# Performance work log

Hardware: AMD Instinct MI355X
Metric: run time of the kernel (lower is better)

Reference implementation:

```python
import jax, jax.numpy as jnp
import numpy as np

T, DIM, H = 1024, 2048, 16
QLR, KVLR = 1024, 512
NOPE, ROPE, VD = 128, 64, 128
QKD = NOPE + ROPE          # 192
IH, ID, TOPK = 16, 128, 256
EPS = 1e-6

def rmsnorm(x, w):
    return x * jax.lax.rsqrt(jnp.mean(x * x, axis=-1, keepdims=True) + EPS) * w

def layernorm(x, w, b, eps=1e-5):
    m = jnp.mean(x, axis=-1, keepdims=True)
    v = jnp.mean((x - m) ** 2, axis=-1, keepdims=True)
    return (x - m) * jax.lax.rsqrt(v + eps) * w + b

def apply_rope(x, cos, sin):
    # non-interleaved: first half = real, second half = imag
    d = x.shape[-1] // 2
    while cos.ndim < x.ndim:
        cos, sin = cos[:, None], sin[:, None]
    x1, x2 = x[..., :d], x[..., d:]
    return jnp.concatenate([x1 * cos - x2 * sin, x1 * sin + x2 * cos], axis=-1)

def hadamard(x):
    # unnormalized Walsh-Hadamard on last dim (power of 2)
    n = x.shape[-1]
    shape = x.shape
    y, h = x, 1
    while h < n:
        y = y.reshape(shape[:-1] + (-1, 2 * h))
        a, b = y[..., :h], y[..., h:]
        y = jnp.concatenate([a + b, a - b], axis=-1)
        h *= 2
    return y.reshape(shape)

def rotate_activation(x):
    # half-swap then Hadamard on each half
    d = x.shape[-1] // 2
    x1, x2 = x[..., :d], x[..., d:]
    return jnp.concatenate([hadamard(x2), hadamard(x1)], axis=-1)

def setup_inputs() -> dict:
    key = jax.random.key(0)
    ks = jax.random.split(key, 10)
    s = 0.02
    w = lambda k, shp: jax.random.normal(k, shp, jnp.float32) * s
    pos = jnp.arange(T, dtype=jnp.float32)
    inv = 1.0 / (10000.0 ** (jnp.arange(0, ROPE, 2, dtype=jnp.float32) / ROPE))
    ang = pos[:, None] * inv[None, :]
    return {
        'hidden_states': jax.random.normal(ks[0], (T, DIM), jnp.float32),
        'rope_cos': jnp.cos(ang), 'rope_sin': jnp.sin(ang),
        'wq_a': w(ks[1], (QLR, DIM)),
        'q_norm_w': jnp.ones((QLR,), jnp.float32),
        'wq_b': w(ks[2], (H * QKD, QLR)),
        'wkv_a': w(ks[3], (KVLR + ROPE, DIM)),
        'kv_norm_w': jnp.ones((KVLR,), jnp.float32),
        'wkv_b': w(ks[4], (H * (NOPE + VD), KVLR)),
        'wo': w(ks[5], (DIM, H * VD)),
        'iq_norm_w': jnp.ones((QLR,), jnp.float32),
        'iwq_b': w(ks[6], (IH * ID, QLR)),
        'iwk': w(ks[7], (IH * ID, DIM)),
        'k_norm_w': jnp.ones((ID,), jnp.float32),
        'k_norm_b': jnp.zeros((ID,), jnp.float32),
        'wproj': w(ks[8], (IH, DIM)),
    }

def reference(hidden_states, rope_cos, rope_sin, wq_a, q_norm_w, wq_b,
              wkv_a, kv_norm_w, wkv_b, wo, iq_norm_w, iwq_b, iwk,
              k_norm_w, k_norm_b, wproj):
    x = hidden_states
    t = x.shape[0]
    qr = x @ wq_a.T                                   # [t, QLR]

    # ---- lightning indexer: top-k causal token selection ----
    iq = (rmsnorm(qr, iq_norm_w) @ iwq_b.T).reshape(t, IH, ID)
    iq = jnp.concatenate([apply_rope(iq[..., :ROPE], rope_cos, rope_sin), iq[..., ROPE:]], -1)
    iq = rotate_activation(iq)
    ik = layernorm((x @ iwk.T).reshape(t, IH, ID), k_norm_w, k_norm_b)
    ik = jnp.concatenate([apply_rope(ik[..., :ROPE], rope_cos, rope_sin), ik[..., ROPE:]], -1)
    ik = rotate_activation(ik)
    w = (x @ wproj.T) * (IH ** -0.5) * (ID ** -0.5)   # [t, IH]
    dots = jax.nn.relu(jnp.einsum('thd,shd->ths', iq, ik)) * w[:, :, None]
    score = dots.sum(axis=1)                          # [t, t]
    rows = jnp.arange(t)
    score = jnp.where(rows[None, :] <= rows[:, None], score, -jnp.inf)
    _, topk_idx = jax.lax.top_k(score, TOPK)          # [t, TOPK]
    valid = topk_idx <= rows[:, None]
    safe_idx = jnp.where(valid, topk_idx, 0)

    # ---- MLA latent projections ----
    q = (rmsnorm(qr, q_norm_w) @ wq_b.T).reshape(t, H, QKD)
    q_nope, q_pe = q[..., :NOPE], q[..., NOPE:]
    q_pe = apply_rope(q_pe, rope_cos, rope_sin)
    kv_a = x @ wkv_a.T                                # [t, KVLR+ROPE]
    kv = rmsnorm(kv_a[:, :KVLR], kv_norm_w)
    k_pe = apply_rope(kv_a[:, KVLR:], rope_cos, rope_sin)
    wkv = wkv_b.reshape(H, NOPE + VD, KVLR)
    w_k, w_v = wkv[:, :NOPE, :], wkv[:, NOPE:, :]
    q_nope_proj = jnp.einsum('thd,hdc->thc', q_nope, w_k)
    q_key = jnp.concatenate([q_nope_proj, q_pe], -1)  # [t, H, KVLR+ROPE]
    kv_key = jnp.concatenate([kv, k_pe], -1)          # [t, KVLR+ROPE]

    # ---- sparse attention over selected indices ----
    sel = kv_key[safe_idx]                            # [t, TOPK, KVLR+ROPE]
    scale = QKD ** -0.5
    logits = jnp.einsum('thc,tkc->thk', q_key, sel) * scale
    logits = jnp.where(valid[:, None, :], logits, -jnp.inf)
    attn = jax.nn.softmax(logits, axis=-1)
    out_latent = jnp.einsum('thk,tkc->thc', attn, sel[..., :KVLR])
    out_v = jnp.einsum('thc,hdc->thd', out_latent, w_v)
    return out_v.reshape(t, H * VD) @ wo.T            # [t, DIM]
```

## Files before the change

kernel.cpp:

```cpp
#include <hip/hip_runtime.h>
#include <hip/hip_bf16.h>
#include <math.h>

#define T_     1024
#define DIM_   2048
#define H_     16
#define QLR_   1024
#define KVLR_  512
#define NOPE_  128
#define ROPE_  64
#define VD_    128
#define QKD_   192
#define IH_    16
#define ID_    128
#define TOPK_  256
#define CKV_   576

#define SCALE_W    0.022097086912079608f
#define SCALE_LOG  0.07216878364870323f

typedef short bfrag __attribute__((ext_vector_type(8)));
typedef float ffrag __attribute__((ext_vector_type(4)));

__device__ __forceinline__ unsigned short f2bf(float f) {
    union { __hip_bfloat16 h; unsigned short u; } c; c.h = __float2bfloat16(f); return c.u;
}
__device__ __forceinline__ float bf2f(unsigned short u) {
    union { unsigned short u; __hip_bfloat16 h; } c; c.u = u; return __bfloat162float(c.h);
}

struct CastSeg { const float* src; unsigned short* hi; unsigned short* lo; };
struct CastDesc { CastSeg seg[6]; int bstart[7]; int nseg; };

__global__ __launch_bounds__(256) void castm_k(CastDesc d)
{
    int b = blockIdx.x, s = 0;
    #pragma unroll
    for (int i = 1; i < 6; ++i) if (i < d.nseg && b >= d.bstart[i]) s = i;
    long base = ((long)(b - d.bstart[s]) * 256 + threadIdx.x) * 4;
    float4 v = *(const float4*)(d.seg[s].src + base);
    ushort4 h4;
    h4.x = f2bf(v.x); h4.y = f2bf(v.y); h4.z = f2bf(v.z); h4.w = f2bf(v.w);
    *(ushort4*)(d.seg[s].hi + base) = h4;
    if (d.seg[s].lo) {
        ushort4 l4;
        l4.x = f2bf(v.x - bf2f(h4.x));
        l4.y = f2bf(v.y - bf2f(h4.y));
        l4.z = f2bf(v.z - bf2f(h4.z));
        l4.w = f2bf(v.w - bf2f(h4.w));
        *(ushort4*)(d.seg[s].lo + base) = l4;
    }
}

__global__ __launch_bounds__(256) void qrnorm_k(const float* __restrict__ qr,
    const float* __restrict__ iqw, const float* __restrict__ qw,
    unsigned short* __restrict__ qriq_hi, unsigned short* __restrict__ qriq_lo,
    unsigned short* __restrict__ qrq_hi)
{
    int t = blockIdx.x, tid = threadIdx.x;
    long base = (long)t * QLR_ + tid * 4;
    float4 v = *(const float4*)(qr + base);
    __shared__ float red[256];
    red[tid] = v.x * v.x + v.y * v.y + v.z * v.z + v.w * v.w;
    __syncthreads();
    for (int off = 128; off; off >>= 1) { if (tid < off) red[tid] += red[tid + off]; __syncthreads(); }
    float r = rsqrtf(red[0] / (float)QLR_ + 1e-6f);
    int col = tid * 4;
    float4 wi = *(const float4*)(iqw + col);
    float4 wq = *(const float4*)(qw + col);
    float s[4] = {v.x, v.y, v.z, v.w};
    float wiv[4] = {wi.x, wi.y, wi.z, wi.w};
    float wqv[4] = {wq.x, wq.y, wq.z, wq.w};
    ushort4 h4, l4, g4;
    unsigned short* hp = (unsigned short*)&h4;
    unsigned short* lp = (unsigned short*)&l4;
    unsigned short* gp = (unsigned short*)&g4;
    #pragma unroll
    for (int i = 0; i < 4; ++i) {
        float ai = s[i] * wiv[i] * r;
        float aq = s[i] * wqv[i] * r;
        hp[i] = f2bf(ai);
        lp[i] = f2bf(ai - bf2f(hp[i]));
        gp[i] = f2bf(aq);
    }
    *(ushort4*)(qriq_hi + base) = h4;
    *(ushort4*)(qriq_lo + base) = l4;
    *(ushort4*)(qrq_hi + base) = g4;
}

__global__ __launch_bounds__(256) void gemm_bt_mfma_k(
    const unsigned short* __restrict__ A, const unsigned short* __restrict__ B,
    void* __restrict__ Cv, long sA, long sB, long sC,
    int lda, int ldb, int ldc, int N, int K, int obf)
{
    A += (long)blockIdx.z * sA;
    B += (long)blockIdx.z * sB;
    __shared__ unsigned short As[128 * 40];
    __shared__ unsigned short Bs[128 * 40];
    const int tid = threadIdx.x;
    const int bm = blockIdx.y * 128, bn = blockIdx.x * 128;
    const int wave = tid >> 6, lane = tid & 63;
    const int wm = (wave >> 1) * 64, wn = (wave & 1) * 64;
    const int lm = lane & 15, quad = lane >> 4;

    ffrag acc[4][4];
    #pragma unroll
    for (int mi = 0; mi < 4; ++mi)
        #pragma unroll
        for (int ni = 0; ni < 4; ++ni)
            #pragma unroll
            for (int r = 0; r < 4; ++r) acc[mi][ni][r] = 0.f;

    const int srow = tid >> 1, shalf = tid & 1;
    const long aoff = (long)(bm + srow) * lda + shalf * 16;
    int brow = bn + srow; if (brow > N - 1) brow = N - 1;
    const long boff = (long)brow * ldb + shalf * 16;
    unsigned short* la = As + srow * 40 + shalf * 16;
    unsigned short* lb = Bs + srow * 40 + shalf * 16;

    uint4 va0 = *(const uint4*)(A + aoff);
    uint4 va1 = *(const uint4*)(A + aoff + 8);
    uint4 vb0 = *(const uint4*)(B + boff);
    uint4 vb1 = *(const uint4*)(B + boff + 8);

    for (int k0 = 0; k0 < K; k0 += 32) {
        __syncthreads();
        *(uint4*)la = va0; *(uint4*)(la + 8) = va1;
        *(uint4*)lb = vb0; *(uint4*)(lb + 8) = vb1;
        __syncthreads();
        if (k0 + 32 < K) {
            va0 = *(const uint4*)(A + aoff + k0 + 32);
            va1 = *(const uint4*)(A + aoff + k0 + 40);
            vb0 = *(const uint4*)(B + boff + k0 + 32);
            vb1 = *(const uint4*)(B + boff + k0 + 40);
        }
        bfrag af[4], bf[4];
        #pragma unroll
        for (int mi = 0; mi < 4; ++mi)
            af[mi] = *(const bfrag*)(As + (wm + mi * 16 + lm) * 40 + quad * 8);
        #pragma unroll
        for (int ni = 0; ni < 4; ++ni)
            bf[ni] = *(const bfrag*)(Bs + (wn + ni * 16 + lm) * 40 + quad * 8);
        #pragma unroll
        for (int mi = 0; mi < 4; ++mi)
            #pragma unroll
            for (int ni = 0; ni < 4; ++ni)
                acc[mi][ni] = __builtin_amdgcn_mfma_f32_16x16x32_bf16(
                    af[mi], bf[ni], acc[mi][ni], 0, 0, 0);
    }

    #pragma unroll
    for (int mi = 0; mi < 4; ++mi)
        #pragma unroll
        for (int ni = 0; ni < 4; ++ni) {
            int n = bn + wn + ni * 16 + lm;
            if (n < N) {
                int mb = bm + wm + mi * 16 + quad * 4;
                if (obf) {
                    unsigned short* C = (unsigned short*)Cv + (long)blockIdx.z * sC;
                    #pragma unroll
                    for (int r = 0; r < 4; ++r)
                        C[(long)(mb + r) * ldc + n] = f2bf(acc[mi][ni][r]);
                } else {
                    float* C = (float*)Cv + (long)blockIdx.z * sC;
                    #pragma unroll
                    for (int r = 0; r < 4; ++r)
                        C[(long)(mb + r) * ldc + n] = acc[mi][ni][r];
                }
            }
        }
}

struct GSeg {
    const void* A; const void* Al; const void* B; const void* Bl;
    void* C; void* C2;
    long sA, sB, sC;
    int lda, ldb, ldc, N, K, bnx, bmx, mode, obf;
};
struct GDesc { GSeg seg[4]; int bstart[5]; int nseg; };

__global__ __launch_bounds__(256) void mgemm_k(GDesc d)
{
    __shared__ unsigned short Ahs[64 * 72], Als[64 * 72], Bhs[64 * 72], Bls[64 * 72];
    const int tid = threadIdx.x;
    const int b = blockIdx.x;
    int s = 0;
    #pragma unroll
    for (int i = 1; i < 4; ++i) if (i < d.nseg && b >= d.bstart[i]) s = i;
    const int rel = b - d.bstart[s];
    const int mode = d.seg[s].mode;

    if (mode == 2) {
        const float* src = (const float*)d.seg[s].A;
        unsigned short* hi = (unsigned short*)d.seg[s].C;
        unsigned short* lo = (unsigned short*)d.seg[s].C2;
        long base = ((long)rel * 256 + tid) * 4;
        float4 v = *(const float4*)(src + base);
        ushort4 h4;
        h4.x = f2bf(v.x); h4.y = f2bf(v.y); h4.z = f2bf(v.z); h4.w = f2bf(v.w);
        *(ushort4*)(hi + base) = h4;
        if (lo) {
            ushort4 l4;
            l4.x = f2bf(v.x - bf2f(h4.x));
            l4.y = f2bf(v.y - bf2f(h4.y));
            l4.z = f2bf(v.z - bf2f(h4.z));
            l4.w = f2bf(v.w - bf2f(h4.w));
            *(ushort4*)(lo + base) = l4;
        }
        return;
    }
    if (mode == 3) {
        const float* x = (const float*)d.seg[s].A;
        const float* wproj = (const float*)d.seg[s].B;
        float* wt = (float*)d.seg[s].C;
        float* xs = (float*)Ahs;
        int t = rel;
        for (int c = tid; c < DIM_; c += 256) xs[c] = x[(long)t * DIM_ + c];
        __syncthreads();
        int wave = tid >> 6, lane = tid & 63;
        #pragma unroll
        for (int i = 0; i < 4; ++i) {
            int h = wave * 4 + i;
            float sum = 0.f;
            for (int c = lane; c < DIM_; c += 64) sum += xs[c] * wproj[(long)h * DIM_ + c];
            for (int off = 32; off; off >>= 1) sum += __shfl_xor(sum, off, 64);
            if (lane == 0) wt[(long)t * IH_ + h] = sum * SCALE_W;
        }
        return;
    }
    if (mode == 4) {
        const float* in = (const float*)d.seg[s].A;
        unsigned short* out = (unsigned short*)d.seg[s].C;
        int h = rel >> 6, c0 = (rel & 15) * 32, d0 = ((rel >> 4) & 3) * 32;
        float (*tt)[33] = (float(*)[33])(void*)Ahs;
        int tx = tid & 31, ty = tid >> 5;
        #pragma unroll
        for (int i = 0; i < 4; ++i)
            tt[ty + i * 8][tx] = in[(long)(h * 256 + d0 + ty + i * 8) * 512 + c0 + tx];
        __syncthreads();
        #pragma unroll
        for (int i = 0; i < 4; ++i)
            out[((long)h * 512 + c0 + ty + i * 8) * 128 + d0 + tx] = f2bf(tt[tx][ty + i * 8]);
        return;
    }
    if (mode == 5) {
        const float* q = (const float*)d.seg[s].A;
        const float* cosb = (const float*)d.seg[s].B;
        const float* sinb = (const float*)d.seg[s].Bl;
        unsigned short* qk = (unsigned short*)d.seg[s].C;
        int row = rel * 8 + (tid >> 5);
        int i = tid & 31;
        int t = row / H_;
        const float* qp = q + (long)row * QKD_ + NOPE_;
        float x1 = qp[i], x2 = qp[i + 32];
        float c = cosb[t * 32 + i], sn = sinb[t * 32 + i];
        unsigned short* o = qk + (long)row * CKV_ + 512;
        o[i]      = f2bf(x1 * c - x2 * sn);
        o[i + 32] = f2bf(x1 * sn + x2 * c);
        return;
    }

    const GSeg g = d.seg[s];
    const bool three = (mode == 1);
    const int per = g.bnx * g.bmx;
    const int z = rel / per;
    const int r2 = rel - z * per;
    const int bm = (r2 / g.bnx) * 64, bn = (r2 % g.bnx) * 64;
    const unsigned short* A  = (const unsigned short*)g.A + (long)z * g.sA;
    const unsigned short* B  = (const unsigned short*)g.B + (long)z * g.sB;
    const unsigned short* Alp = (const unsigned short*)g.Al;
    const unsigned short* Blp = (const unsigned short*)g.Bl;

    const int wave = tid >> 6, lane = tid & 63;
    const int wm = (wave >> 1) * 32, wn = (wave & 1) * 32;
    const int lm = lane & 15, quad = lane >> 4;

    ffrag acc[2][2];
    #pragma unroll
    for (int mi = 0; mi < 2; ++mi)
        #pragma unroll
        for (int ni = 0; ni < 2; ++ni)
            #pragma unroll
            for (int r = 0; r < 4; ++r) acc[mi][ni][r] = 0.f;

    const int srow = tid >> 2, schunk = tid & 3;
    const long aoff = (long)(bm + srow) * g.lda + schunk * 8;
    int brow = bn + srow; if (brow > g.N - 1) brow = g.N - 1;
    const long boff = (long)brow * g.ldb + schunk * 8;
    const int loff = srow * 72 + schunk * 8;

    uint4 va0, va1, vb0, vb1, wa0, wa1, wb0, wb1;
    va0 = *(const uint4*)(A + aoff);
    va1 = *(const uint4*)(A + aoff + 32);
    vb0 = *(const uint4*)(B + boff);
    vb1 = *(const uint4*)(B + boff + 32);
    if (three) {
        wa0 = *(const uint4*)(Alp + aoff);
        wa1 = *(const uint4*)(Alp + aoff + 32);
        wb0 = *(const uint4*)(Blp + boff);
        wb1 = *(const uint4*)(Blp + boff + 32);
    }

    for (int k0 = 0; k0 < g.K; k0 += 64) {
        __syncthreads();
        *(uint4*)(Ahs + loff) = va0; *(uint4*)(Ahs + loff + 32) = va1;
        *(uint4*)(Bhs + loff) = vb0; *(uint4*)(Bhs + loff + 32) = vb1;
        if (three) {
            *(uint4*)(Als + loff) = wa0; *(uint4*)(Als + loff + 32) = wa1;
            *(uint4*)(Bls + loff) = wb0; *(uint4*)(Bls + loff + 32) = wb1;
        }
        __syncthreads();
        if (k0 + 64 < g.K) {
            va0 = *(const uint4*)(A + aoff + k0 + 64);
            va1 = *(const uint4*)(A + aoff + k0 + 96);
            vb0 = *(const uint4*)(B + boff + k0 + 64);
            vb1 = *(const uint4*)(B + boff + k0 + 96);
            if (three) {
                wa0 = *(const uint4*)(Alp + aoff + k0 + 64);
                wa1 = *(const uint4*)(Alp + aoff + k0 + 96);
                wb0 = *(const uint4*)(Blp + boff + k0 + 64);
                wb1 = *(const uint4*)(Blp + boff + k0 + 96);
            }
        }
        bfrag ah[2][2], bh[2][2], al[2][2], bl[2][2];
        #pragma unroll
        for (int mi = 0; mi < 2; ++mi)
            #pragma unroll
            for (int ks = 0; ks < 2; ++ks)
                ah[mi][ks] = *(const bfrag*)(Ahs + (wm + mi * 16 + lm) * 72 + ks * 32 + quad * 8);
        #pragma unroll
        for (int ni = 0; ni < 2; ++ni)
            #pragma unroll
            for (int ks = 0; ks < 2; ++ks)
                bh[ni][ks] = *(const bfrag*)(Bhs + (wn + ni * 16 + lm) * 72 + ks * 32 + quad * 8);
        if (three) {
            #pragma unroll
            for (int mi = 0; mi < 2; ++mi)
                #pragma unroll
                for (int ks = 0; ks < 2; ++ks)
                    al[mi][ks] = *(const bfrag*)(Als + (wm + mi * 16 + lm) * 72 + ks * 32 + quad * 8);
            #pragma unroll
            for (int ni = 0; ni < 2; ++ni)
                #pragma unroll
                for (int ks = 0; ks < 2; ++ks)
                    bl[ni][ks] = *(const bfrag*)(Bls + (wn + ni * 16 + lm) * 72 + ks * 32 + quad * 8);
        }
        #pragma unroll
        for (int mi = 0; mi < 2; ++mi)
            #pragma unroll
            for (int ni = 0; ni < 2; ++ni) {
                acc[mi][ni] = __builtin_amdgcn_mfma_f32_16x16x32_bf16(ah[mi][0], bh[ni][0], acc[mi][ni], 0, 0, 0);
                if (three) {
                    acc[mi][ni] = __builtin_amdgcn_mfma_f32_16x16x32_bf16(ah[mi][0], bl[ni][0], acc[mi][ni], 0, 0, 0);
                    acc[mi][ni] = __builtin_amdgcn_mfma_f32_16x16x32_bf16(al[mi][0], bh[ni][0], acc[mi][ni], 0, 0, 0);
                }
                acc[mi][ni] = __builtin_amdgcn_mfma_f32_16x16x32_bf16(ah[mi][1], bh[ni][1], acc[mi][ni], 0, 0, 0);
                if (three) {
                    acc[mi][ni] = __builtin_amdgcn_mfma_f32_16x16x32_bf16(ah[mi][1], bl[ni][1], acc[mi][ni], 0, 0, 0);
                    acc[mi][ni] = __builtin_amdgcn_mfma_f32_16x16x32_bf16(al[mi][1], bh[ni][1], acc[mi][ni], 0, 0, 0);
                }
            }
    }

    #pragma unroll
    for (int mi = 0; mi < 2; ++mi)
        #pragma unroll
        for (int ni = 0; ni < 2; ++ni) {
            int n = bn + wn + ni * 16 + lm;
            if (n < g.N) {
                int mb = bm + wm + mi * 16 + quad * 4;
                if (g.obf) {
                    unsigned short* C = (unsigned short*)g.C + (long)z * g.sC;
                    #pragma unroll
                    for (int r = 0; r < 4; ++r)
                        C[(long)(mb + r) * g.ldc + n] = f2bf(acc[mi][ni][r]);
                } else {
                    float* C = (float*)g.C + (long)z * g.sC;
                    #pragma unroll
                    for (int r = 0; r < 4; ++r)
                        C[(long)(mb + r) * g.ldc + n] = acc[mi][ni][r];
                }
            }
        }
}

__global__ __launch_bounds__(256) void mtrans_k(
    const float* __restrict__ iq, unsigned short* __restrict__ iqh, unsigned short* __restrict__ iql,
    const float* __restrict__ ik, unsigned short* __restrict__ ikh, unsigned short* __restrict__ ikl,
    const float* __restrict__ knw, const float* __restrict__ knb,
    const float* __restrict__ kva, unsigned short* __restrict__ kvb, const float* __restrict__ kvnw,
    const float* __restrict__ cosb, const float* __restrict__ sinb)
{
    __shared__ float red[256];
    __shared__ float rsh;
    const int b = blockIdx.x, tid = threadIdx.x;
    if (b < 8192) {
        const bool isq = b < 4096;
        int rb = isq ? b : b - 4096;
        int row = rb * 4 + (tid >> 6);
        int p = tid & 63;
        int t = row >> 4;
        const float* src = isq ? iq : ik;
        float a = src[(long)row * 128 + p];
        float bb = src[(long)row * 128 + 64 + p];
        if (!isq) {
            float ssum = a + bb;
            #pragma unroll
            for (int o = 1; o < 64; o <<= 1) ssum += __shfl_xor(ssum, o, 64);
            float m = ssum * (1.f / 128.f);
            float da = a - m, db = bb - m;
            float v = da * da + db * db;
            #pragma unroll
            for (int o = 1; o < 64; o <<= 1) v += __shfl_xor(v, o, 64);
            float r = rsqrtf(v * (1.f / 128.f) + 1e-5f);
            a = da * r * knw[p] + knb[p];
            bb = db * r * knw[64 + p] + knb[64 + p];
        }
        float c = cosb[t * 32 + (p & 31)], sn = sinb[t * 32 + (p & 31)];
        float asw = __shfl_xor(a, 32, 64);
        a = (p < 32) ? (a * c - asw * sn) : (asw * sn + a * c);
        #pragma unroll
        for (int h = 1; h < 64; h <<= 1) {
            float a2 = __shfl_xor(a, h, 64);
            float b2 = __shfl_xor(bb, h, 64);
            a = (p & h) ? (a2 - a) : (a + a2);
            bb = (p & h) ? (b2 - bb) : (bb + b2);
        }
        unsigned short* hi = isq ? iqh : ikh;
        unsigned short* lo = isq ? iql : ikl;
        unsigned short hb = f2bf(bb), ha = f2bf(a);
        hi[(long)row * 128 + p] = hb;
        hi[(long)row * 128 + 64 + p] = ha;
        lo[(long)row * 128 + p] = f2bf(bb - bf2f(hb));
        lo[(long)row * 128 + 64 + p] = f2bf(a - bf2f(ha));
    } else {
        int t = b - 8192;
        const float* a = kva + (long)t * CKV_;
        unsigned short* o = kvb + (long)t * CKV_;
        float v0 = a[tid], v1 = a[tid + 256];
        red[tid] = v0 * v0 + v1 * v1; __syncthreads();
        for (int off = 128; off; off >>= 1) { if (tid < off) red[tid] += red[tid + off]; __syncthreads(); }
        if (tid == 0) rsh = rsqrtf(red[0] / (float)KVLR_ + 1e-6f);
        __syncthreads();
        float rs = rsh;
        o[tid]       = f2bf(v0 * rs * kvnw[tid]);
        o[tid + 256] = f2bf(v1 * rs * kvnw[tid + 256]);
        if (tid < 32) {
            float x1 = a[512 + tid], x2 = a[544 + tid];
            float c = cosb[t * 32 + tid], sn = sinb[t * 32 + tid];
            o[512 + tid] = f2bf(x1 * c - x2 * sn);
            o[544 + tid] = f2bf(x1 * sn + x2 * c);
        }
    }
}

__global__ __launch_bounds__(256) void score3_k(
    const unsigned short* __restrict__ iqh, const unsigned short* __restrict__ iql,
    const unsigned short* __restrict__ ikh, const unsigned short* __restrict__ ikl,
    const float* __restrict__ wtok, float* __restrict__ score)
{
    const int bt = blockIdx.y, bs = blockIdx.x;
    if (bs > bt) return;
    __shared__ unsigned short Ah[64 * 72], Al[64 * 72], Bh[64 * 72], Bl[64 * 72];
    __shared__ float wts[64][16];
    const int tid = threadIdx.x;
    const int wave = tid >> 6, lane = tid & 63;
    const int wm = (wave >> 1) * 32, wn = (wave & 1) * 32;
    const int lm = lane & 15, quad = lane >> 4;
    const int t0 = bt * 64, s0 = bs * 64;
    const int srow = tid >> 2, schunk = tid & 3;
    const int loff = srow * 72 + schunk * 8;

    for (int e = tid; e < 1024; e += 256)
        wts[e >> 4][e & 15] = wtok[(long)(t0 + (e >> 4)) * IH_ + (e & 15)];

    const long abase = (long)(t0 + srow) * 2048 + schunk * 8;
    const long bbase = (long)(s0 + srow) * 2048 + schunk * 8;

    uint4 pah0 = *(const uint4*)(iqh + abase);
    uint4 pah1 = *(const uint4*)(iqh + abase + 32);
    uint4 pal0 = *(const uint4*)(iql + abase);
    uint4 pal1 = *(const uint4*)(iql + abase + 32);
    uint4 pbh0 = *(const uint4*)(ikh + bbase);
    uint4 pbh1 = *(const uint4*)(ikh + bbase + 32);
    uint4 pbl0 = *(const uint4*)(ikl + bbase);
    uint4 pbl1 = *(const uint4*)(ikl + bbase + 32);

    float accf[2][2][4] = {};

    for (int h = 0; h < IH_; ++h) {
        ffrag acch[2][2];
        #pragma unroll
        for (int mi = 0; mi < 2; ++mi)
            #pragma unroll
            for (int ni = 0; ni < 2; ++ni)
                #pragma unroll
                for (int r = 0; r < 4; ++r) acch[mi][ni][r] = 0.f;

        #pragma unroll
        for (int k0 = 0; k0 < ID_; k0 += 64) {
            __syncthreads();
            *(uint4*)(Ah + loff) = pah0; *(uint4*)(Ah + loff + 32) = pah1;
            *(uint4*)(Al + loff) = pal0; *(uint4*)(Al + loff + 32) = pal1;
            *(uint4*)(Bh + loff) = pbh0; *(uint4*)(Bh + loff + 32) = pbh1;
            *(uint4*)(Bl + loff) = pbl0; *(uint4*)(Bl + loff + 32) = pbl1;
            __syncthreads();
            int step = h * 2 + (k0 >> 6) + 1;
            if (step < 32) {
                int off = (step >> 1) * 128 + (step & 1) * 64;
                pah0 = *(const uint4*)(iqh + abase + off);
                pah1 = *(const uint4*)(iqh + abase + off + 32);
                pal0 = *(const uint4*)(iql + abase + off);
                pal1 = *(const uint4*)(iql + abase + off + 32);
                pbh0 = *(const uint4*)(ikh + bbase + off);
                pbh1 = *(const uint4*)(ikh + bbase + off + 32);
                pbl0 = *(const uint4*)(ikl + bbase + off);
                pbl1 = *(const uint4*)(ikl + bbase + off + 32);
            }
            bfrag ahf[2][2], alf[2][2], bhf[2][2], blf[2][2];
            #pragma unroll
            for (int mi = 0; mi < 2; ++mi)
                #pragma unroll
                for (int ks = 0; ks < 2; ++ks) {
                    ahf[mi][ks] = *(const bfrag*)(Ah + (wm + mi * 16 + lm) * 72 + ks * 32 + quad * 8);
                    alf[mi][ks] = *(const bfrag*)(Al + (wm + mi * 16 + lm) * 72 + ks * 32 + quad * 8);
                }
            #pragma unroll
            for (int ni = 0; ni < 2; ++ni)
                #pragma unroll
                for (int ks = 0; ks < 2; ++ks) {
                    bhf[ni][ks] = *(const bfrag*)(Bh + (wn + ni * 16 + lm) * 72 + ks * 32 + quad * 8);
                    blf[ni][ks] = *(const bfrag*)(Bl + (wn + ni * 16 + lm) * 72 + ks * 32 + quad * 8);
                }
            #pragma unroll
            for (int mi = 0; mi < 2; ++mi)
                #pragma unroll
                for (int ni = 0; ni < 2; ++ni) {
                    acch[mi][ni] = __builtin_amdgcn_mfma_f32_16x16x32_bf16(ahf[mi][0], bhf[ni][0], acch[mi][ni], 0, 0, 0);
                    acch[mi][ni] = __builtin_amdgcn_mfma_f32_16x16x32_bf16(ahf[mi][0], blf[ni][0], acch[mi][ni], 0, 0, 0);
                    acch[mi][ni] = __builtin_amdgcn_mfma_f32_16x16x32_bf16(alf[mi][0], bhf[ni][0], acch[mi][ni], 0, 0, 0);
                    acch[mi][ni] = __builtin_amdgcn_mfma_f32_16x16x32_bf16(ahf[mi][1], bhf[ni][1], acch[mi][ni], 0, 0, 0);
                    acch[mi][ni] = __builtin_amdgcn_mfma_f32_16x16x32_bf16(ahf[mi][1], blf[ni][1], acch[mi][ni], 0, 0, 0);
                    acch[mi][ni] = __builtin_amdgcn_mfma_f32_16x16x32_bf16(alf[mi][1], bhf[ni][1], acch[mi][ni], 0, 0, 0);
                }
        }
        #pragma unroll
        for (int mi = 0; mi < 2; ++mi) {
            float wr[4];
            #pragma unroll
            for (int r = 0; r < 4; ++r) wr[r] = wts[wm + mi * 16 + quad * 4 + r][h];
            #pragma unroll
            for (int ni = 0; ni < 2; ++ni)
                #pragma unroll
                for (int r = 0; r < 4; ++r)
                    accf[mi][ni][r] += fmaxf(acch[mi][ni][r], 0.f) * wr[r];
        }
    }
    #pragma unroll
    for (int mi = 0; mi < 2; ++mi)
        #pragma unroll
        for (int ni = 0; ni < 2; ++ni) {
            int s = s0 + wn + ni * 16 + lm;
            int tb = t0 + wm + mi * 16 + quad * 4;
            #pragma unroll
            for (int r = 0; r < 4; ++r)
                score[(long)(tb + r) * T_ + s] = accf[mi][ni][r];
        }
}

__global__ __launch_bounds__(512) void topk_k(const float* __restrict__ score, int* __restrict__ topk)
{
    int t = blockIdx.x, tid = threadIdx.x;
    __shared__ float v[1024];
    __shared__ int ix[1024];
    for (int i = tid; i < 1024; i += 512) {
        v[i] = (i <= t) ? score[(long)t * T_ + i] : -INFINITY;
        ix[i] = i;
    }
    __syncthreads();
    for (int k = 2; k <= 1024; k <<= 1) {
        for (int j = k >> 1; j > 0; j >>= 1) {
            for (int i = tid; i < 1024; i += 512) {
                int l = i ^ j;
                if (l > i) {
                    bool up = ((i & k) == 0);
                    float vi = v[i], vl = v[l];
                    int xi = ix[i], xl = ix[l];
                    bool iBetter = (vi > vl) || (vi == vl && xi < xl);
                    bool doSwap = up ? !iBetter : iBetter;
                    if (doSwap) { v[i] = vl; v[l] = vi; ix[i] = xl; ix[l] = xi; }
                }
            }
            __syncthreads();
        }
    }
    if (tid < 256) topk[(long)t * TOPK_ + tid] = ix[tid];
}

__global__ __launch_bounds__(256, 4) void attn3_k(
    const unsigned short* __restrict__ qkeyb, const unsigned short* __restrict__ kvb,
    const int* __restrict__ topkp, unsigned short* __restrict__ olat)
{
    __shared__ __align__(16) unsigned short U[13568];
    __shared__ float red[16 * 17];
    __shared__ int kidx[256];
    unsigned short* Qbf = U;
    float*          Lg  = (float*)U;
    unsigned short* VT0 = U;
    unsigned short* VT1 = U + 4608;
    unsigned short* Pbf = U + 9344;

    const int t = blockIdx.x, tid = threadIdx.x;
    const int wave = tid >> 6, lane = tid & 63;
    const int lm = lane & 15, quad = lane >> 4;

    kidx[tid] = topkp[(long)t * TOPK_ + tid];
    const uint2* q2 = (const uint2*)(qkeyb + (long)t * (H_ * CKV_));
    #pragma unroll
    for (int rep = 0; rep < 9; ++rep) {
        int e = rep * 256 + tid;
        uint2 v = q2[e];
        int f = e * 4, h = f / CKV_, c = f - h * CKV_;
        *(uint2*)(Qbf + h * 584 + c) = v;
    }
    int myk0 = topkp[(long)t * TOPK_ + wave * 64 + 0 * 16 + lm];
    int myk1 = topkp[(long)t * TOPK_ + wave * 64 + 1 * 16 + lm];
    int myk2 = topkp[(long)t * TOPK_ + wave * 64 + 2 * 16 + lm];
    int myk3 = topkp[(long)t * TOPK_ + wave * 64 + 3 * 16 + lm];
    __syncthreads();

    ffrag acc[4];
    #pragma unroll
    for (int ni = 0; ni < 4; ++ni)
        #pragma unroll
        for (int r = 0; r < 4; ++r) acc[ni][r] = 0.f;

    const unsigned short* kb0 = kvb + (long)myk0 * CKV_ + quad * 8;
    const unsigned short* kb1 = kvb + (long)myk1 * CKV_ + quad * 8;
    const unsigned short* kb2 = kvb + (long)myk2 * CKV_ + quad * 8;
    const unsigned short* kb3 = kvb + (long)myk3 * CKV_ + quad * 8;

    bfrag ba[4], bb[4], bc[4];
    #define LDT(DST, C) { \
        DST[0] = *(const bfrag*)(kb0 + (C)); \
        DST[1] = *(const bfrag*)(kb1 + (C)); \
        DST[2] = *(const bfrag*)(kb2 + (C)); \
        DST[3] = *(const bfrag*)(kb3 + (C)); }
    #define PHA_STEP(I, BUF) { \
        bfrag af = *(const bfrag*)(Qbf + lm * 584 + (I) * 32 + quad * 8); \
        _Pragma("unroll") \
        for (int ni = 0; ni < 4; ++ni) \
            acc[ni] = __builtin_amdgcn_mfma_f32_16x16x32_bf16(af, BUF[ni], acc[ni], 0, 0, 0); \
        if ((I) < 15) LDT(BUF, (I) * 32 + 96) }

    LDT(ba, 0) LDT(bb, 32) LDT(bc, 64)
    PHA_STEP(0, ba)  PHA_STEP(1, bb)  PHA_STEP(2, bc)
    PHA_STEP(3, ba)  PHA_STEP(4, bb)  PHA_STEP(5, bc)
    PHA_STEP(6, ba)  PHA_STEP(7, bb)  PHA_STEP(8, bc)
    PHA_STEP(9, ba)  PHA_STEP(10, bb) PHA_STEP(11, bc)
    PHA_STEP(12, ba) PHA_STEP(13, bb) PHA_STEP(14, bc)
    PHA_STEP(15, ba) PHA_STEP(16, bb) PHA_STEP(17, bc)
    #undef PHA_STEP
    #undef LDT

    __syncthreads();
    #pragma unroll
    for (int ni = 0; ni < 4; ++ni)
        #pragma unroll
        for (int r = 0; r < 4; ++r)
            Lg[(quad * 4 + r) * 260 + wave * 64 + ni * 16 + lm] = acc[ni][r];
    __syncthreads();

    {
        int h = tid >> 4, j = tid & 15;
        float m = -INFINITY;
        #pragma unroll
        for (int kk = 0; kk < 16; ++kk) {
            int key = j * 16 + kk;
            if (kidx[key] <= t) m = fmaxf(m, Lg[h * 260 + key]);
        }
        red[h * 17 + j] = m;
        __syncthreads();
        float mh = -INFINITY;
        #pragma unroll
        for (int jj = 0; jj < 16; ++jj) mh = fmaxf(mh, red[h * 17 + jj]);
        __syncthreads();
        float s = 0.f;
        float pv[16];
        #pragma unroll
        for (int kk = 0; kk < 16; ++kk) {
            int key = j * 16 + kk;
            float e = (kidx[key] <= t) ? expf(Lg[h * 260 + key] * SCALE_LOG - mh * SCALE_LOG) : 0.f;
            pv[kk] = e; s += e;
        }
        red[h * 17 + j] = s;
        __syncthreads();
        float sh = 0.f;
        #pragma unroll
        for (int jj = 0; jj < 16; ++jj) sh += red[h * 17 + jj];
        float inv = 1.f / sh;
        #pragma unroll
        for (int kk = 0; kk < 16; ++kk)
            Pbf[h * 264 + j * 16 + kk] = f2bf(pv[kk] * inv);
    }

    const int kpair = tid & 15, cgrp = tid >> 4;
    ffrag acc2[2];
    #pragma unroll
    for (int ci = 0; ci < 2; ++ci)
        #pragma unroll
        for (int r = 0; r < 4; ++r) acc2[ci][r] = 0.f;

    uint4 ga0, gb0, ga1, gb1;
    #define PREFB(GA, GB, IT) { \
        int ka_ = kidx[((IT) & 7) * 32 + 2 * kpair]; \
        int kb_ = kidx[((IT) & 7) * 32 + 2 * kpair + 1]; \
        long co_ = (long)(((IT) >> 3) * 128 + cgrp * 8); \
        GA = *(const uint4*)(kvb + (long)ka_ * CKV_ + co_); \
        GB = *(const uint4*)(kvb + (long)kb_ * CKV_ + co_); }
    #define STOREB(GA, GB, BUF) { \
        const unsigned short* pa_ = (const unsigned short*)&GA; \
        const unsigned short* pb_ = (const unsigned short*)&GB; \
        _Pragma("unroll") \
        for (int i_ = 0; i_ < 8; ++i_) \
            *(unsigned int*)((BUF) + (cgrp * 8 + i_) * 36 + 2 * kpair) = \
                (unsigned int)pa_[i_] | ((unsigned int)pb_[i_] << 16); }
    #define MFMAB(BUF, IT) { \
        bfrag pa = *(const bfrag*)(Pbf + lm * 264 + ((IT) & 7) * 32 + quad * 8); \
        _Pragma("unroll") \
        for (int ci = 0; ci < 2; ++ci) { \
            int c = wave * 32 + ci * 16 + lm; \
            bfrag bv; \
            ((uint2*)&bv)[0] = *(const uint2*)((BUF) + c * 36 + quad * 8); \
            ((uint2*)&bv)[1] = *(const uint2*)((BUF) + c * 36 + quad * 8 + 4); \
            acc2[ci] = __builtin_amdgcn_mfma_f32_16x16x32_bf16(pa, bv, acc2[ci], 0, 0, 0); } }
    #define OLATST(IT) { \
        int p_ = (IT) >> 3; \
        _Pragma("unroll") \
        for (int ci = 0; ci < 2; ++ci) \
            _Pragma("unroll") \
            for (int r = 0; r < 4; ++r) \
                olat[((long)t * H_ + quad * 4 + r) * 512 + p_ * 128 + wave * 32 + ci * 16 + lm] \
                    = f2bf(acc2[ci][r]); \
        _Pragma("unroll") \
        for (int ci = 0; ci < 2; ++ci) \
            _Pragma("unroll") \
            for (int r = 0; r < 4; ++r) acc2[ci][r] = 0.f; }
    #define LGKBAR() { asm volatile("s_waitcnt lgkmcnt(0)" ::: "memory"); \
                       __builtin_amdgcn_s_barrier(); }

    PREFB(ga0, gb0, 0);
    PREFB(ga1, gb1, 1);
    LGKBAR();
    STOREB(ga0, gb0, VT0);
    LGKBAR();
    for (int it = 0; it < 32; it += 2) {
        STOREB(ga1, gb1, VT1);
        MFMAB(VT0, it);
        if (it + 2 < 32) PREFB(ga0, gb0, it + 2);
        LGKBAR();
        if (it + 2 < 32) STOREB(ga0, gb0, VT0);
        MFMAB(VT1, it + 1);
        if (it + 3 < 32) PREFB(ga1, gb1, it + 3);
        if (((it + 1) & 7) == 7) OLATST(it + 1);
        LGKBAR();
    }
    #undef PREFB
    #undef STOREB
    #undef MFMAB
    #undef OLATST
    #undef LGKBAR
}

extern "C" void kernel_launch(void* const* d_in, const int* in_sizes, int n_in,
                              void* d_out, int out_size, void* d_ws, size_t ws_size,
                              hipStream_t stream)
{
    const float* x          = (const float*)d_in[0];
    const float* cosb       = (const float*)d_in[1];
    const float* sinb       = (const float*)d_in[2];
    const float* wq_a       = (const float*)d_in[3];
    const float* q_norm_w   = (const float*)d_in[4];
    const float* wq_b       = (const float*)d_in[5];
    const float* wkv_a      = (const float*)d_in[6];
    const float* kv_norm_w  = (const float*)d_in[7];
    const float* wkv_b      = (const float*)d_in[8];
    const float* wo         = (const float*)d_in[9];
    const float* iq_norm_w  = (const float*)d_in[10];
    const float* iwq_b      = (const float*)d_in[11];
    const float* iwk        = (const float*)d_in[12];
    const float* k_norm_w   = (const float*)d_in[13];
    const float* k_norm_b   = (const float*)d_in[14];
    const float* wproj      = (const float*)d_in[15];
    float* out = (float*)d_out;

    float* ws    = (float*)d_ws;
    float* qr    = ws;
    float* wtok  = ws + 1049600;
    int*   topk  = (int*)(ws + 1655808);
    float* qkey  = ws + 1917952;
    float* outv  = ws + 11355136;
    float* U0    = ws + 13452288;
    float* iq    = U0;
    float* ik    = U0 + 2097152;
    float* kva   = U0 + 4194304;
    float* qbuf  = U0 + 4784128;
    float* score = U0 + 7929856;

    unsigned short* qkey_u = (unsigned short*)qkey;
    unsigned short* wqa_hi  = qkey_u;
    unsigned short* wqa_lo  = qkey_u + 2097152;
    unsigned short* iwk_hi  = qkey_u + 4194304;
    unsigned short* iwk_lo  = qkey_u + 8388608;
    unsigned short* iwqb_hi = qkey_u + 12582912;
    unsigned short* iwqb_lo = qkey_u + 14680064;
    unsigned short* qriq_hi = qkey_u + 16777216;
    unsigned short* qriq_lo = qkey_u + 17825792;
    unsigned short* iqbf_hi = qkey_u;
    unsigned short* iqbf_lo = qkey_u + 2097152;
    unsigned short* ikbf_hi = qkey_u + 4194304;
    unsigned short* ikbf_lo = qkey_u + 6291456;
    unsigned short* qkey_bf = qkey_u;
    unsigned short* wkvb_bf = qkey_u + 9437184;
    unsigned short* wo_bf   = qkey_u;
    unsigned short* q_u     = (unsigned short*)qbuf;
    unsigned short* x_hi    = q_u;
    unsigned short* x_lo    = q_u + 2097152;
    unsigned short* wkva_hi = q_u + 4194304;
    unsigned short* outv_u  = (unsigned short*)outv;
    unsigned short* wqb_hi  = outv_u;
    unsigned short* qrq_hi  = outv_u + 3145728;
    unsigned short* outv_bf = outv_u;
    unsigned short* qbf     = (unsigned short*)iq;
    unsigned short* wkT     = (unsigned short*)ik;
    unsigned short* kvb     = (unsigned short*)qr;
    unsigned short* olat_bf = (unsigned short*)U0;

    {
        CastDesc d;
        d.seg[0] = { x,      x_hi,    x_lo    };
        d.seg[1] = { wq_a,   wqa_hi,  wqa_lo  };
        d.seg[2] = { iwk,    iwk_hi,  iwk_lo  };
        d.seg[3] = { iwq_b,  iwqb_hi, iwqb_lo };
        d.seg[4] = { wkv_a,  wkva_hi, nullptr };
        d.seg[5] = { wq_b,   wqb_hi,  nullptr };
        d.bstart[0] = 0;     d.bstart[1] = 2048;  d.bstart[2] = 4096;
        d.bstart[3] = 8192;  d.bstart[4] = 10240; d.bstart[5] = 11392;
        d.bstart[6] = 14464; d.nseg = 6;
        castm_k<<<14464, 256, 0, stream>>>(d);
    }

    {
        GDesc d{};
        d.nseg = 3;
        d.bstart[0] = 0; d.bstart[1] = 256; d.bstart[2] = 768; d.bstart[3] = 1792;
        GSeg& s0 = d.seg[0];
        s0.A = x_hi; s0.Al = x_lo; s0.B = wqa_hi; s0.Bl = wqa_lo; s0.C = qr;
        s0.lda = DIM_; s0.ldb = DIM_; s0.ldc = QLR_; s0.N = QLR_; s0.K = DIM_;
        s0.bnx = 16; s0.bmx = 16; s0.mode = 1; s0.obf = 0;
        GSeg& s1 = d.seg[1];
        s1.A = x_hi; s1.Al = x_lo; s1.B = iwk_hi; s1.Bl = iwk_lo; s1.C = ik;
        s1.lda = DIM_; s1.ldb = DIM_; s1.ldc = IH_ * ID_; s1.N = IH_ * ID_; s1.K = DIM_;
        s1.bnx = 32; s1.bmx = 16; s1.mode = 1; s1.obf = 0;
        GSeg& s2 = d.seg[2];
        s2.A = x; s2.B = wproj; s2.C = wtok; s2.mode = 3;
        mgemm_k<<<1792, 256, 0, stream>>>(d);
    }

    qrnorm_k<<<T_, 256, 0, stream>>>(qr, iq_norm_w, q_norm_w, qriq_hi, qriq_lo, qrq_hi);

    {
        GDesc d{};
        d.nseg = 3;
        d.bstart[0] = 0; d.bstart[1] = 512; d.bstart[2] = 656; d.bstart[3] = 2704;
        GSeg& s0 = d.seg[0];
        s0.A = qriq_hi; s0.Al = qriq_lo; s0.B = iwqb_hi; s0.Bl = iwqb_lo; s0.C = iq;
        s0.lda = QLR_; s0.ldb = QLR_; s0.ldc = IH_ * ID_; s0.N = IH_ * ID_; s0.K = QLR_;
        s0.bnx = 32; s0.bmx = 16; s0.mode = 1; s0.obf = 0;
        GSeg& s1 = d.seg[1];
        s1.A = x_hi; s1.B = wkva_hi; s1.C = kva;
        s1.lda = DIM_; s1.ldb = DIM_; s1.ldc = CKV_; s1.N = CKV_; s1.K = DIM_;
        s1.bnx = 9; s1.bmx = 16; s1.mode = 0; s1.obf = 0;
        GSeg& s2 = d.seg[2];
        s2.A = wkv_b; s2.C = wkvb_bf; s2.C2 = nullptr; s2.mode = 2;
        mgemm_k<<<2704, 256, 0, stream>>>(d);
    }

    {
        GDesc d{};
        d.nseg = 1;
        d.bstart[0] = 0; d.bstart[1] = 768;
        GSeg& s0 = d.seg[0];
        s0.A = qrq_hi; s0.B = wqb_hi; s0.C = qbuf;
        s0.lda = QLR_; s0.ldb = QLR_; s0.ldc = H_ * QKD_; s0.N = H_ * QKD_; s0.K = QLR_;
        s0.bnx = 48; s0.bmx = 16; s0.mode = 0; s0.obf = 0;
        mgemm_k<<<768, 256, 0, stream>>>(d);
    }

    mtrans_k<<<9216, 256, 0, stream>>>(iq, iqbf_hi, iqbf_lo, ik, ikbf_hi, ikbf_lo,
                                       k_norm_w, k_norm_b, kva, kvb, kv_norm_w, cosb, sinb);

    score3_k<<<dim3(T_/64, T_/64), 256, 0, stream>>>(iqbf_hi, iqbf_lo, ikbf_hi, ikbf_lo, wtok, score);
    topk_k<<<T_, 512, 0, stream>>>(score, topk);

    {
        GDesc d{};
        d.nseg = 3;
        d.bstart[0] = 0; d.bstart[1] = 3072; d.bstart[2] = 4096; d.bstart[3] = 6144;
        GSeg& s0 = d.seg[0];
        s0.A = qbuf; s0.C = qbf; s0.C2 = nullptr; s0.mode = 2;
        GSeg& s1 = d.seg[1];
        s1.A = wkv_b; s1.C = wkT; s1.mode = 4;
        GSeg& s2 = d.seg[2];
        s2.A = qbuf; s2.B = cosb; s2.Bl = sinb; s2.C = qkey_bf; s2.mode = 5;
        mgemm_k<<<6144, 256, 0, stream>>>(d);
    }

    gemm_bt_mfma_k<<<dim3(KVLR_/128, T_/128, H_), 256, 0, stream>>>(
        qbf, wkT, qkey_bf, 192L, 65536L, 576L, H_*QKD_, ID_, H_*CKV_, KVLR_, ID_, 1);

    attn3_k<<<T_, 256, 0, stream>>>(qkey_bf, kvb, topk, olat_bf);

    {
        GDesc d{};
        d.nseg = 2;
        d.bstart[0] = 0; d.bstart[1] = 512; d.bstart[2] = 4608;
        GSeg& s0 = d.seg[0];
        s0.A = olat_bf; s0.B = wkvb_bf + (long)NOPE_ * KVLR_; s0.C = outv_bf;
        s0.sA = 512; s0.sB = (long)(NOPE_ + VD_) * KVLR_; s0.sC = VD_;
        s0.lda = H_ * KVLR_; s0.ldb = KVLR_; s0.ldc = H_ * VD_; s0.N = VD_; s0.K = KVLR_;
        s0.bnx = 2; s0.bmx = 16; s0.mode = 0; s0.obf = 1;
        GSeg& s1 = d.seg[1];
        s1.A = wo; s1.C = wo_bf; s1.C2 = nullptr; s1.mode = 2;
        mgemm_k<<<4608, 256, 0, stream>>>(d);
    }

    {
        GDesc d{};
        d.nseg = 1;
        d.bstart[0] = 0; d.bstart[1] = 512;
        GSeg& s0 = d.seg[0];
        s0.A = outv_bf; s0.B = wo_bf; s0.C = out;
        s0.lda = H_ * VD_; s0.ldb = H_ * VD_; s0.ldc = DIM_; s0.N = DIM_; s0.K = H_ * VD_;
        s0.bnx = 32; s0.bmx = 16; s0.mode = 0; s0.obf = 0;
        mgemm_k<<<512, 256, 0, stream>>>(d);
    }

    (void)in_sizes; (void)n_in; (void)out_size; (void)ws_size;
}
```

Measured before the change: 494.3 us.

## Split indexer score kernel across head groups and sum partials in top-k

The indexer score kernel gains a grid z-dimension of 4, so each block handles 4 of the 16 indexer heads. Each block writes a partial score plane, and the top-k kernel sums the four partial planes while loading its row. The aim is to fill the GPU better: before, only the lower-triangular 136 tiles of a 16x16 grid did any work. In exchange the kernel writes and reads four score planes instead of one, reuses the now-dead iq/ik workspace for them, and changes the float summation order.

```diff
diff --git a/kernel.cpp b/kernel.cpp
--- a/kernel.cpp
+++ b/kernel.cpp
@@ -457,10 +457,13 @@
 __global__ __launch_bounds__(256) void score3_k(
     const unsigned short* __restrict__ iqh, const unsigned short* __restrict__ iql,
     const unsigned short* __restrict__ ikh, const unsigned short* __restrict__ ikl,
-    const float* __restrict__ wtok, float* __restrict__ score)
+    const float* __restrict__ wtok, float* __restrict__ scorep)
 {
     const int bt = blockIdx.y, bs = blockIdx.x;
     if (bs > bt) return;
+    const int hz = blockIdx.z;
+    const int h0 = hz * 4;
+    float* score = scorep + (long)hz * (T_ * T_);
     __shared__ unsigned short Ah[64 * 72], Al[64 * 72], Bh[64 * 72], Bl[64 * 72];
     __shared__ float wts[64][16];
     const int tid = threadIdx.x;
@@ -474,8 +477,8 @@
     for (int e = tid; e < 1024; e += 256)
         wts[e >> 4][e & 15] = wtok[(long)(t0 + (e >> 4)) * IH_ + (e & 15)];
 
-    const long abase = (long)(t0 + srow) * 2048 + schunk * 8;
-    const long bbase = (long)(s0 + srow) * 2048 + schunk * 8;
+    const long abase = (long)(t0 + srow) * 2048 + schunk * 8 + h0 * 128;
+    const long bbase = (long)(s0 + srow) * 2048 + schunk * 8 + h0 * 128;
 
     uint4 pah0 = *(const uint4*)(iqh + abase);
     uint4 pah1 = *(const uint4*)(iqh + abase + 32);
@@ -488,7 +491,8 @@
 
     float accf[2][2][4] = {};
 
-    for (int h = 0; h < IH_; ++h) {
+    for (int hh = 0; hh < 4; ++hh) {
+        const int h = h0 + hh;
         ffrag acch[2][2];
         #pragma unroll
         for (int mi = 0; mi < 2; ++mi)
@@ -505,9 +509,9 @@
             *(uint4*)(Bh + loff) = pbh0; *(uint4*)(Bh + loff + 32) = pbh1;
             *(uint4*)(Bl + loff) = pbl0; *(uint4*)(Bl + loff + 32) = pbl1;
             __syncthreads();
-            int step = h * 2 + (k0 >> 6) + 1;
-            if (step < 32) {
-                int off = (step >> 1) * 128 + (step & 1) * 64;
+            int step = hh * 2 + (k0 >> 6) + 1;
+            if (step < 8) {
+                long off = (long)(step >> 1) * 128 + (step & 1) * 64;
                 pah0 = *(const uint4*)(iqh + abase + off);
                 pah1 = *(const uint4*)(iqh + abase + off + 32);
                 pal0 = *(const uint4*)(iql + abase + off);
@@ -568,13 +572,17 @@
         }
 }
 
-__global__ __launch_bounds__(512) void topk_k(const float* __restrict__ score, int* __restrict__ topk)
+__global__ __launch_bounds__(512) void topk_k(const float* __restrict__ scorep, int* __restrict__ topk)
 {
     int t = blockIdx.x, tid = threadIdx.x;
     __shared__ float v[1024];
     __shared__ int ix[1024];
+    const float* p0 = scorep + (long)t * T_;
+    const float* p1 = p0 + (long)1 * T_ * T_;
+    const float* p2 = p0 + (long)2 * T_ * T_;
+    const float* p3 = p0 + (long)3 * T_ * T_;
     for (int i = tid; i < 1024; i += 512) {
-        v[i] = (i <= t) ? score[(long)t * T_ + i] : -INFINITY;
+        v[i] = (i <= t) ? (p0[i] + p1[i] + p2[i] + p3[i]) : -INFINITY;
         ix[i] = i;
     }
     __syncthreads();
@@ -805,7 +813,7 @@
     float* ik    = U0 + 2097152;
     float* kva   = U0 + 4194304;
     float* qbuf  = U0 + 4784128;
-    float* score = U0 + 7929856;
+    float* scorep = U0;
 
     unsigned short* qkey_u = (unsigned short*)qkey;
     unsigned short* wqa_hi  = qkey_u;
@@ -900,8 +908,8 @@
     mtrans_k<<<9216, 256, 0, stream>>>(iq, iqbf_hi, iqbf_lo, ik, ikbf_hi, ikbf_lo,
                                        k_norm_w, k_norm_b, kva, kvb, kv_norm_w, cosb, sinb);
 
-    score3_k<<<dim3(T_/64, T_/64), 256, 0, stream>>>(iqbf_hi, iqbf_lo, ikbf_hi, ikbf_lo, wtok, score);
-    topk_k<<<T_, 512, 0, stream>>>(score, topk);
+    score3_k<<<dim3(T_/64, T_/64, 4), 256, 0, stream>>>(iqbf_hi, iqbf_lo, ikbf_hi, ikbf_lo, wtok, scorep);
+    topk_k<<<T_, 512, 0, stream>>>(scorep, topk);
 
     {
         GDesc d{};
```

Measured after the change: 493.4 us, median of 2. No clear change (-0.2%).
